# Performance work log

Hardware: AMD Instinct MI355X
Metric: run time of the kernel (lower is better)

## Reference

```python
import jax, jax.numpy as jnp
import numpy as np


def setup_inputs() -> dict:
    key = jax.random.key(0)
    k1, k2 = jax.random.split(key)
    B, N = 1024, 4096
    protein_coords_pred = jax.random.normal(k1, (B, N, 3), dtype=jnp.float32) * 10.0
    protein_coords = jax.random.normal(k2, (B, N, 3), dtype=jnp.float32) * 10.0
    return {"protein_coords_pred": protein_coords_pred, "protein_coords": protein_coords}


def reference(protein_coords_pred, protein_coords):
    # protein_coords_pred, protein_coords: [B, N, 3]
    pred_mean = jnp.mean(protein_coords_pred, axis=1, keepdims=True)   # [B,1,3]
    true_mean = jnp.mean(protein_coords, axis=1, keepdims=True)        # [B,1,3]
    pred_c = protein_coords_pred - pred_mean                           # [B,N,3]
    true_c = protein_coords - true_mean                                # [B,N,3]

    # Cross-covariance A = pred_c^T @ true_c : [B,3,3]
    A = jnp.einsum('bni,bnj->bij', pred_c, true_c)
    U, S, Vt = jnp.linalg.svd(A)                                       # batched 3x3 SVD

    # sign(det(Vt^T @ U^T)) == sign(det(U) * det(Vt))
    d = jnp.sign(jnp.linalg.det(U) * jnp.linalg.det(Vt))               # [B]
    corr = jnp.stack([jnp.ones_like(d), jnp.ones_like(d), d], axis=-1) # [B,3]
    # rotation = U @ diag(1,1,d) @ Vt : scale U's columns then matmul
    rotation = jnp.einsum('bik,bkj->bij', U * corr[:, None, :], Vt)    # [B,3,3]

    # aligned true coords = (true - true_mean) @ R^T + pred_mean
    aligned = jnp.einsum('bij,bnj->bni', rotation, true_c) + pred_mean # [B,N,3]

    sq = jnp.sum((protein_coords_pred - aligned) ** 2, axis=-1)        # [B,N]
    rmsds = jnp.sqrt(jnp.mean(sq, axis=-1))                            # [B]
    return jnp.mean(rmsds)
```

## Files before the change

kernel.cpp:

```cpp
#include <hip/hip_runtime.h>
#include <math.h>

#define N_PTS 4096
#define FB (N_PTS * 3)
#define BLK 256
#define SPLIT 4
#define PPB (N_PTS / SPLIT)
#define F4PB (PPB * 3 / 4)
#define STATS 17

__device__ inline float wave_reduce_sum_f32(float v) {
    #pragma unroll
    for (int off = 32; off > 0; off >>= 1) v += __shfl_xor(v, off, 64);
    return v;
}

__global__ __launch_bounds__(BLK) void kabsch_reduce(const float4* __restrict__ pred4,
                                                     const float4* __restrict__ tru4,
                                                     float* __restrict__ ws, int nblocks) {
    __shared__ float4 sm[2 * F4PB];
    const int bid = blockIdx.x, tid = threadIdx.x;
    const int b = bid >> 2, h = bid & 3;
    const size_t base = (size_t)b * (FB / 4) + (size_t)h * F4PB;

    float4 rp0 = pred4[base + 0 * BLK + tid];
    float4 rp1 = pred4[base + 1 * BLK + tid];
    float4 rp2 = pred4[base + 2 * BLK + tid];
    float4 rt0 = tru4 [base + 0 * BLK + tid];
    float4 rt1 = tru4 [base + 1 * BLK + tid];
    float4 rt2 = tru4 [base + 2 * BLK + tid];
    sm[0 * BLK + tid] = rp0;
    sm[1 * BLK + tid] = rp1;
    sm[2 * BLK + tid] = rp2;
    sm[F4PB + 0 * BLK + tid] = rt0;
    sm[F4PB + 1 * BLK + tid] = rt1;
    sm[F4PB + 2 * BLK + tid] = rt2;
    __syncthreads();

    const float* smp = reinterpret_cast<const float*>(&sm[0]);
    const float* smt = reinterpret_cast<const float*>(&sm[F4PB]);
    const float4* pp = reinterpret_cast<const float4*>(smp + tid * 12);
    const float4* tt = reinterpret_cast<const float4*>(smt + tid * 12);
    float4 p0 = pp[0], p1 = pp[1], p2 = pp[2];
    float4 t0 = tt[0], t1 = tt[1], t2 = tt[2];

    float a[STATS];
    #pragma unroll
    for (int i = 0; i < STATS; ++i) a[i] = 0.0f;

#define ACC(px, py, pz, tx, ty, tz) do {                                        \
        a[0] += (px); a[1] += (py); a[2] += (pz);                               \
        a[3] += (tx); a[4] += (ty); a[5] += (tz);                               \
        a[6] = fmaf((px),(px), fmaf((py),(py), fmaf((pz),(pz), a[6])));         \
        a[7] = fmaf((tx),(tx), fmaf((ty),(ty), fmaf((tz),(tz), a[7])));         \
        a[8]  = fmaf((px),(tx), a[8]);  a[9]  = fmaf((px),(ty), a[9]);          \
        a[10] = fmaf((px),(tz), a[10]); a[11] = fmaf((py),(tx), a[11]);         \
        a[12] = fmaf((py),(ty), a[12]); a[13] = fmaf((py),(tz), a[13]);         \
        a[14] = fmaf((pz),(tx), a[14]); a[15] = fmaf((pz),(ty), a[15]);         \
        a[16] = fmaf((pz),(tz), a[16]);                                         \
    } while (0)

    ACC(p0.x, p0.y, p0.z, t0.x, t0.y, t0.z);
    ACC(p0.w, p1.x, p1.y, t0.w, t1.x, t1.y);
    ACC(p1.z, p1.w, p2.x, t1.z, t1.w, t2.x);
    ACC(p2.y, p2.z, p2.w, t2.y, t2.z, t2.w);
#undef ACC

    #pragma unroll
    for (int i = 0; i < STATS; ++i) {
        a[i] += __shfl_xor(a[i], 1, 64);
        a[i] += __shfl_xor(a[i], 2, 64);
    }

    __syncthreads();
    float* tl = reinterpret_cast<float*>(sm);
    const int grp = tid >> 2, sub = tid & 3;
    #pragma unroll
    for (int k = 0; k < 5; ++k) {
        const int s = sub + 4 * k;
        if (s < STATS) tl[s * 68 + grp] = a[s];
    }
    __syncthreads();
    if (tid < STATS) {
        const float4* row = reinterpret_cast<const float4*>(&tl[tid * 68]);
        float4 acc4 = row[0];
        #pragma unroll
        for (int k = 1; k < BLK / 16; ++k) {
            float4 v = row[k];
            acc4.x += v.x; acc4.y += v.y; acc4.z += v.z; acc4.w += v.w;
        }
        ws[(size_t)tid * nblocks + bid] = (acc4.x + acc4.y) + (acc4.z + acc4.w);
    }
}

__global__ __launch_bounds__(1024) void kabsch_finalize(const float* __restrict__ ws,
                                                        float* __restrict__ out,
                                                        int B, int nblocks) {
    const int tid = threadIdx.x;
    float rmsd = 0.0f;
    if (tid < B) {
        float w[STATS];
        #pragma unroll
        for (int s = 0; s < STATS; ++s) {
            float4 v = *reinterpret_cast<const float4*>(&ws[(size_t)s * nblocks + tid * SPLIT]);
            w[s] = (v.x + v.y) + (v.z + v.w);
        }
        const float invN = 1.0f / (float)N_PTS;
        float sp[3] = {w[0], w[1], w[2]};
        float st[3] = {w[3], w[4], w[5]};
        float A[3][3];
        #pragma unroll
        for (int i = 0; i < 3; ++i)
            #pragma unroll
            for (int j = 0; j < 3; ++j)
                A[i][j] = w[8 + i * 3 + j] - sp[i] * st[j] * invN;
        float Sp = w[6] - (sp[0] * sp[0] + sp[1] * sp[1] + sp[2] * sp[2]) * invN;
        float St = w[7] - (st[0] * st[0] + st[1] * st[1] + st[2] * st[2]) * invN;

        float detA = A[0][0] * (A[1][1] * A[2][2] - A[1][2] * A[2][1])
                   - A[0][1] * (A[1][0] * A[2][2] - A[1][2] * A[2][0])
                   + A[0][2] * (A[1][0] * A[2][1] - A[1][1] * A[2][0]);

        float G00 = A[0][0]*A[0][0] + A[1][0]*A[1][0] + A[2][0]*A[2][0];
        float G11 = A[0][1]*A[0][1] + A[1][1]*A[1][1] + A[2][1]*A[2][1];
        float G22 = A[0][2]*A[0][2] + A[1][2]*A[1][2] + A[2][2]*A[2][2];
        float G01 = A[0][0]*A[0][1] + A[1][0]*A[1][1] + A[2][0]*A[2][1];
        float G02 = A[0][0]*A[0][2] + A[1][0]*A[1][2] + A[2][0]*A[2][2];
        float G12 = A[0][1]*A[0][2] + A[1][1]*A[1][2] + A[2][1]*A[2][2];

        float q = (G00 + G11 + G22) * (1.0f / 3.0f);
        float p1 = G01 * G01 + G02 * G02 + G12 * G12;
        float b00 = G00 - q, b11 = G11 - q, b22 = G22 - q;
        float p2 = b00 * b00 + b11 * b11 + b22 * b22 + 2.0f * p1;
        float p = sqrtf(p2 * (1.0f / 6.0f));
        float e1, e2, e3;
        if (p > 1e-30f + 1e-6f * fabsf(q)) {
            float ip = 1.0f / p;
            float C00 = b00 * ip, C11 = b11 * ip, C22 = b22 * ip;
            float C01 = G01 * ip, C02 = G02 * ip, C12 = G12 * ip;
            float r = 0.5f * (C00 * (C11 * C22 - C12 * C12)
                            - C01 * (C01 * C22 - C12 * C02)
                            + C02 * (C01 * C12 - C11 * C02));
            r = fminf(1.0f, fmaxf(-1.0f, r));
            float phi = acosf(r) * (1.0f / 3.0f);
            e1 = q + 2.0f * p * __cosf(phi);
            e3 = q + 2.0f * p * __cosf(phi + 2.0943951023931953f);
            e2 = 3.0f * q - e1 - e3;
        } else {
            e1 = e2 = e3 = q;
        }
        float s1 = sqrtf(fmaxf(e1, 0.0f));
        float s2 = sqrtf(fmaxf(e2, 0.0f));
        float s3 = sqrtf(fmaxf(e3, 0.0f));
        float d = (detA < 0.0f) ? -1.0f : 1.0f;
        float tr = s1 + s2 + d * s3;
        float msd = (Sp + St - 2.0f * tr) * invN;
        rmsd = sqrtf(fmaxf(msd, 0.0f));
    }

    rmsd = wave_reduce_sum_f32(rmsd);
    __shared__ float red[16];
    const int lane = tid & 63, wid = tid >> 6;
    if (lane == 0) red[wid] = rmsd;
    __syncthreads();
    if (tid == 0) {
        float tot = 0.0f;
        #pragma unroll
        for (int w = 0; w < 16; ++w) tot += red[w];
        out[0] = tot / (float)B;
    }
}

extern "C" void kernel_launch(void* const* d_in, const int* in_sizes, int n_in,
                              void* d_out, int out_size, void* d_ws, size_t ws_size,
                              hipStream_t stream) {
    const float4* pred4 = (const float4*)d_in[0];
    const float4* tru4  = (const float4*)d_in[1];
    float* out = (float*)d_out;
    float* ws = (float*)d_ws;
    const int B = in_sizes[0] / FB;
    const int nblocks = B * SPLIT;

    kabsch_reduce<<<dim3(nblocks), dim3(BLK), 0, stream>>>(pred4, tru4, ws, nblocks);
    kabsch_finalize<<<dim3(1), dim3(1024), 0, stream>>>(ws, out, B, nblocks);
}
```

Measured before the change: 27.46 us.

## Process each batch in one block with staged prefetch and per-block SVD finalize

Each block now handles a whole batch element, looping over four stages. The next stage's global loads are prefetched into registers while the current stage is staged through shared memory, and the block computes its own 3x3 eigen-solve and RMSD. The second kernel shrinks to a small mean over B values. This spreads the serial per-batch finalize across all blocks instead of one 1024-thread block and removes the workspace round trip, but it cuts grid size fourfold (1024 blocks instead of 4096) and adds two barriers per stage. The mean kernel assumes B equals 1024 with 256 threads reading float4.

New measurement: 25.40 us. 1.08x faster.

```diff
diff --git a/kernel.cpp b/kernel.cpp
--- a/kernel.cpp
+++ b/kernel.cpp
@@ -3,10 +3,10 @@
 
 #define N_PTS 4096
 #define FB (N_PTS * 3)
+#define F4B (FB / 4)
 #define BLK 256
-#define SPLIT 4
-#define PPB (N_PTS / SPLIT)
-#define F4PB (PPB * 3 / 4)
+#define STAGES 4
+#define F4S (F4B / STAGES)
 #define STATS 17
 
 __device__ inline float wave_reduce_sum_f32(float v) {
@@ -15,13 +15,12 @@
     return v;
 }
 
-__global__ __launch_bounds__(BLK) void kabsch_reduce(const float4* __restrict__ pred4,
-                                                     const float4* __restrict__ tru4,
-                                                     float* __restrict__ ws, int nblocks) {
-    __shared__ float4 sm[2 * F4PB];
-    const int bid = blockIdx.x, tid = threadIdx.x;
-    const int b = bid >> 2, h = bid & 3;
-    const size_t base = (size_t)b * (FB / 4) + (size_t)h * F4PB;
+__global__ __launch_bounds__(BLK) void kabsch_batch(const float4* __restrict__ pred4,
+                                                    const float4* __restrict__ tru4,
+                                                    float* __restrict__ rmsds) {
+    __shared__ float4 sm[2 * F4S];
+    const int b = blockIdx.x, tid = threadIdx.x;
+    const size_t base = (size_t)b * F4B;
 
     float4 rp0 = pred4[base + 0 * BLK + tid];
     float4 rp1 = pred4[base + 1 * BLK + tid];
@@ -29,20 +28,6 @@
     float4 rt0 = tru4 [base + 0 * BLK + tid];
     float4 rt1 = tru4 [base + 1 * BLK + tid];
     float4 rt2 = tru4 [base + 2 * BLK + tid];
-    sm[0 * BLK + tid] = rp0;
-    sm[1 * BLK + tid] = rp1;
-    sm[2 * BLK + tid] = rp2;
-    sm[F4PB + 0 * BLK + tid] = rt0;
-    sm[F4PB + 1 * BLK + tid] = rt1;
-    sm[F4PB + 2 * BLK + tid] = rt2;
-    __syncthreads();
-
-    const float* smp = reinterpret_cast<const float*>(&sm[0]);
-    const float* smt = reinterpret_cast<const float*>(&sm[F4PB]);
-    const float4* pp = reinterpret_cast<const float4*>(smp + tid * 12);
-    const float4* tt = reinterpret_cast<const float4*>(smt + tid * 12);
-    float4 p0 = pp[0], p1 = pp[1], p2 = pp[2];
-    float4 t0 = tt[0], t1 = tt[1], t2 = tt[2];
 
     float a[STATS];
     #pragma unroll
@@ -60,10 +45,36 @@
         a[16] = fmaf((pz),(tz), a[16]);                                         \
     } while (0)
 
-    ACC(p0.x, p0.y, p0.z, t0.x, t0.y, t0.z);
-    ACC(p0.w, p1.x, p1.y, t0.w, t1.x, t1.y);
-    ACC(p1.z, p1.w, p2.x, t1.z, t1.w, t2.x);
-    ACC(p2.y, p2.z, p2.w, t2.y, t2.z, t2.w);
+    #pragma unroll
+    for (int s = 0; s < STAGES; ++s) {
+        sm[0 * BLK + tid] = rp0;
+        sm[1 * BLK + tid] = rp1;
+        sm[2 * BLK + tid] = rp2;
+        sm[F4S + 0 * BLK + tid] = rt0;
+        sm[F4S + 1 * BLK + tid] = rt1;
+        sm[F4S + 2 * BLK + tid] = rt2;
+        if (s < STAGES - 1) {
+            const size_t nb = base + (size_t)(s + 1) * F4S;
+            rp0 = pred4[nb + 0 * BLK + tid];
+            rp1 = pred4[nb + 1 * BLK + tid];
+            rp2 = pred4[nb + 2 * BLK + tid];
+            rt0 = tru4 [nb + 0 * BLK + tid];
+            rt1 = tru4 [nb + 1 * BLK + tid];
+            rt2 = tru4 [nb + 2 * BLK + tid];
+        }
+        __syncthreads();
+        const float* smp = reinterpret_cast<const float*>(&sm[0]);
+        const float* smt = reinterpret_cast<const float*>(&sm[F4S]);
+        const float4* pp = reinterpret_cast<const float4*>(smp + tid * 12);
+        const float4* tt = reinterpret_cast<const float4*>(smt + tid * 12);
+        float4 p0 = pp[0], p1 = pp[1], p2 = pp[2];
+        float4 t0 = tt[0], t1 = tt[1], t2 = tt[2];
+        ACC(p0.x, p0.y, p0.z, t0.x, t0.y, t0.z);
+        ACC(p0.w, p1.x, p1.y, t0.w, t1.x, t1.y);
+        ACC(p1.z, p1.w, p2.x, t1.z, t1.w, t2.x);
+        ACC(p2.y, p2.z, p2.w, t2.y, t2.z, t2.w);
+        __syncthreads();
+    }
 #undef ACC
 
     #pragma unroll
@@ -71,8 +82,6 @@
         a[i] += __shfl_xor(a[i], 1, 64);
         a[i] += __shfl_xor(a[i], 2, 64);
     }
-
-    __syncthreads();
     float* tl = reinterpret_cast<float*>(sm);
     const int grp = tid >> 2, sub = tid & 3;
     #pragma unroll
@@ -81,6 +90,7 @@
         if (s < STATS) tl[s * 68 + grp] = a[s];
     }
     __syncthreads();
+    float* fin = tl + STATS * 68;
     if (tid < STATS) {
         const float4* row = reinterpret_cast<const float4*>(&tl[tid * 68]);
         float4 acc4 = row[0];
@@ -89,22 +99,14 @@
             float4 v = row[k];
             acc4.x += v.x; acc4.y += v.y; acc4.z += v.z; acc4.w += v.w;
         }
-        ws[(size_t)tid * nblocks + bid] = (acc4.x + acc4.y) + (acc4.z + acc4.w);
+        fin[tid] = (acc4.x + acc4.y) + (acc4.z + acc4.w);
     }
-}
-
-__global__ __launch_bounds__(1024) void kabsch_finalize(const float* __restrict__ ws,
-                                                        float* __restrict__ out,
-                                                        int B, int nblocks) {
-    const int tid = threadIdx.x;
-    float rmsd = 0.0f;
-    if (tid < B) {
+    __syncthreads();
+    if (tid == 0) {
         float w[STATS];
         #pragma unroll
-        for (int s = 0; s < STATS; ++s) {
-            float4 v = *reinterpret_cast<const float4*>(&ws[(size_t)s * nblocks + tid * SPLIT]);
-            w[s] = (v.x + v.y) + (v.z + v.w);
-        }
+        for (int i = 0; i < STATS; ++i) w[i] = fin[i];
+
         const float invN = 1.0f / (float)N_PTS;
         float sp[3] = {w[0], w[1], w[2]};
         float st[3] = {w[3], w[4], w[5]};
@@ -155,20 +157,21 @@
         float d = (detA < 0.0f) ? -1.0f : 1.0f;
         float tr = s1 + s2 + d * s3;
         float msd = (Sp + St - 2.0f * tr) * invN;
-        rmsd = sqrtf(fmaxf(msd, 0.0f));
+        rmsds[b] = sqrtf(fmaxf(msd, 0.0f));
     }
+}
 
-    rmsd = wave_reduce_sum_f32(rmsd);
-    __shared__ float red[16];
-    const int lane = tid & 63, wid = tid >> 6;
-    if (lane == 0) red[wid] = rmsd;
+__global__ __launch_bounds__(BLK) void kabsch_mean(const float* __restrict__ rmsds,
+                                                   float* __restrict__ out, int B) {
+    const int tid = threadIdx.x;
+    const float4* r4 = reinterpret_cast<const float4*>(rmsds);
+    float4 v = r4[tid];
+    float s = (v.x + v.y) + (v.z + v.w);
+    s = wave_reduce_sum_f32(s);
+    __shared__ float red[4];
+    if ((tid & 63) == 0) red[tid >> 6] = s;
     __syncthreads();
-    if (tid == 0) {
-        float tot = 0.0f;
-        #pragma unroll
-        for (int w = 0; w < 16; ++w) tot += red[w];
-        out[0] = tot / (float)B;
-    }
+    if (tid == 0) out[0] = ((red[0] + red[1]) + (red[2] + red[3])) / (float)B;
 }
 
 extern "C" void kernel_launch(void* const* d_in, const int* in_sizes, int n_in,
@@ -177,10 +180,9 @@
     const float4* pred4 = (const float4*)d_in[0];
     const float4* tru4  = (const float4*)d_in[1];
     float* out = (float*)d_out;
-    float* ws = (float*)d_ws;
+    float* rmsds = (float*)d_ws;
     const int B = in_sizes[0] / FB;
-    const int nblocks = B * SPLIT;
 
-    kabsch_reduce<<<dim3(nblocks), dim3(BLK), 0, stream>>>(pred4, tru4, ws, nblocks);
-    kabsch_finalize<<<dim3(1), dim3(1024), 0, stream>>>(ws, out, B, nblocks);
+    kabsch_batch<<<dim3(B), dim3(BLK), 0, stream>>>(pred4, tru4, rmsds);
+    kabsch_mean<<<dim3(1), dim3(BLK), 0, stream>>>(rmsds, out, B);
 }
```
